# Optimization experiments

Hardware: AMD Instinct MI355X
Metric: run time of the kernel (lower is better)

Reference implementation:

```python
import jax, jax.numpy as jnp
import numpy as np

S, B, K = 64, 16, 512
QD, KD, A = 512, 512, 256


def setup_inputs() -> dict:
    key = jax.random.key(0)
    ks = jax.random.split(key, 10)
    inv_q = 1.0 / np.sqrt(QD)
    inv_k = 1.0 / np.sqrt(KD)
    inv_a = 1.0 / np.sqrt(A)
    return {
        "queries": jax.random.normal(ks[0], (S, B, QD), dtype=jnp.float32),
        "keys": jax.random.normal(ks[1], (B, K, KD), dtype=jnp.float32),
        "null_mask": jax.random.randint(ks[2], (B, K), 0, 2).astype(jnp.bool_),
        # nn.Linear params (PyTorch layout: weight (out, in), bias (out,))
        "Ww": jax.random.uniform(ks[3], (A, QD), jnp.float32, -inv_q, inv_q),
        "Wb": jax.random.uniform(ks[4], (A,), jnp.float32, -inv_q, inv_q),
        "Uw": jax.random.uniform(ks[5], (A, KD), jnp.float32, -inv_k, inv_k),
        "Ub": jax.random.uniform(ks[6], (A,), jnp.float32, -inv_k, inv_k),
        "vw": jax.random.uniform(ks[7], (1, A), jnp.float32, -inv_a, inv_a),
        "vb": jax.random.uniform(ks[8], (1,), jnp.float32, -inv_a, inv_a),
    }


def reference(queries, keys, null_mask, Ww, Wb, Uw, Ub, vw, vb):
    # t_query: (S, B, A); t_key: (B, K, A)
    t_query = jnp.einsum("sbq,aq->sba", queries, Ww) + Wb
    t_key = jnp.einsum("bkd,ad->bka", keys, Uw) + Ub
    # broadcast add -> (S, B, K, A), tanh, project with v -> alpha (S, B, K)
    h = jnp.tanh(t_query[:, :, None, :] + t_key[None, :, :, :])
    alpha = jnp.einsum("sbka,a->sbk", h, vw[0]) + vb[0]
    alpha = jnp.where(null_mask[None, :, :], -jnp.inf, alpha)
    att_weight = jax.nn.softmax(alpha, axis=2)  # (S, B, K)
    # bmm(att_weight^T, keys)^T -> (S, B, KD)
    attened_keys = jnp.einsum("sbk,bkd->sbd", att_weight, keys)
    return attened_keys, alpha
```

## Files before the change

kernel.cpp:

```cpp
#include <hip/hip_runtime.h>
#include <math.h>

#define S_DIM 64
#define B_DIM 16
#define K_DIM 512
#define QD_DIM 512
#define A_DIM 256

#define NEG_BIG (-3.0e38f)

#define SC 2.8853900817779268f

#define TQ_OFF 262144
#define W_WS_OFF ((size_t)2359296)

typedef __attribute__((ext_vector_type(8))) short short8v;
typedef __attribute__((ext_vector_type(4))) float f32x4;

static __device__ __forceinline__ uint2 pack_hi4(float4 v) {
    unsigned x0 = __float_as_uint(v.x), x1 = __float_as_uint(v.y),
             x2 = __float_as_uint(v.z), x3 = __float_as_uint(v.w);
    uint2 r;
    r.x = (x1 & 0xffff0000u) | (x0 >> 16);
    r.y = (x3 & 0xffff0000u) | (x2 >> 16);
    return r;
}
static __device__ __forceinline__ uint2 pack_lo4(float4 v) {
    float l0 = v.x - __uint_as_float(__float_as_uint(v.x) & 0xffff0000u);
    float l1 = v.y - __uint_as_float(__float_as_uint(v.y) & 0xffff0000u);
    float l2 = v.z - __uint_as_float(__float_as_uint(v.z) & 0xffff0000u);
    float l3 = v.w - __uint_as_float(__float_as_uint(v.w) & 0xffff0000u);
    unsigned y0 = __float_as_uint(l0), y1 = __float_as_uint(l1),
             y2 = __float_as_uint(l2), y3 = __float_as_uint(l3);
    uint2 r;
    r.x = (y1 & 0xffff0000u) | (y0 >> 16);
    r.y = (y3 & 0xffff0000u) | (y2 >> 16);
    return r;
}

__global__ __launch_bounds__(256) void lin_mfma(
    const float* __restrict__ queries, const float* __restrict__ keys,
    const float* __restrict__ Ww, const float* __restrict__ Wb,
    const float* __restrict__ Uw, const float* __restrict__ Ub,
    float* __restrict__ t_ws)
{
    __shared__ unsigned short Ah[64][40], Al[64][40], Bh[64][40], Bl[64][40];

    const int bx = blockIdx.x;
    const bool isQ = (bx < 64);
    int mt, nt;
    if (isQ) { mt = bx >> 2; nt = bx & 3; }
    else     { int t = bx - 64; mt = t >> 7; nt = t & 127; }

    const float* __restrict__ Abase = isQ ? queries : Uw;
    const float* __restrict__ Bbase = isQ ? Ww : keys;
    const size_t Aoff = (size_t)(mt * 64) * 512;
    const size_t Boff = (size_t)(nt * 64) * 512;

    const int tid  = threadIdx.x;
    const int srow = tid >> 2;
    const int scol = (tid & 3) << 3;
    const int lane = tid & 63, wid = tid >> 6;
    const int wm = (wid >> 1) << 5, wn = (wid & 1) << 5;
    const int fr  = lane & 15;
    const int fkb = (lane >> 4) << 3;

    f32x4 acc[2][2] = {};

    const float* Ap = Abase + Aoff + (size_t)srow * 512 + scol;
    const float* Bp = Bbase + Boff + (size_t)srow * 512 + scol;

    float4 ra0 = *(const float4*)(Ap);
    float4 ra1 = *(const float4*)(Ap + 4);
    float4 rb0 = *(const float4*)(Bp);
    float4 rb1 = *(const float4*)(Bp + 4);

    for (int ks = 0; ks < 16; ++ks) {
        uint2 ah0 = pack_hi4(ra0), ah1 = pack_hi4(ra1);
        uint2 al0 = pack_lo4(ra0), al1 = pack_lo4(ra1);
        uint2 bh0 = pack_hi4(rb0), bh1 = pack_hi4(rb1);
        uint2 bl0 = pack_lo4(rb0), bl1 = pack_lo4(rb1);
        __syncthreads();
        { uint4 v = {ah0.x, ah0.y, ah1.x, ah1.y}; *(uint4*)&Ah[srow][scol] = v; }
        { uint4 v = {al0.x, al0.y, al1.x, al1.y}; *(uint4*)&Al[srow][scol] = v; }
        { uint4 v = {bh0.x, bh0.y, bh1.x, bh1.y}; *(uint4*)&Bh[srow][scol] = v; }
        { uint4 v = {bl0.x, bl0.y, bl1.x, bl1.y}; *(uint4*)&Bl[srow][scol] = v; }
        __syncthreads();
        if (ks < 15) {
            const int o = (ks + 1) * 32;
            ra0 = *(const float4*)(Ap + o);
            ra1 = *(const float4*)(Ap + o + 4);
            rb0 = *(const float4*)(Bp + o);
            rb1 = *(const float4*)(Bp + o + 4);
        }
        short8v bhv[2], blv[2];
        #pragma unroll
        for (int j = 0; j < 2; ++j) {
            bhv[j] = *(const short8v*)&Bh[wn + j * 16 + fr][fkb];
            blv[j] = *(const short8v*)&Bl[wn + j * 16 + fr][fkb];
        }
        #pragma unroll
        for (int i = 0; i < 2; ++i) {
            short8v ah = *(const short8v*)&Ah[wm + i * 16 + fr][fkb];
            short8v al = *(const short8v*)&Al[wm + i * 16 + fr][fkb];
            #pragma unroll
            for (int j = 0; j < 2; ++j) {
                acc[i][j] = __builtin_amdgcn_mfma_f32_16x16x32_bf16(ah, bhv[j], acc[i][j], 0, 0, 0);
                acc[i][j] = __builtin_amdgcn_mfma_f32_16x16x32_bf16(ah, blv[j], acc[i][j], 0, 0, 0);
                acc[i][j] = __builtin_amdgcn_mfma_f32_16x16x32_bf16(al, bhv[j], acc[i][j], 0, 0, 0);
            }
        }
    }

    const int crow = (lane >> 4) << 2;
    if (isQ) {
        #pragma unroll
        for (int j = 0; j < 2; ++j) {
            const int a_col = nt * 64 + wn + j * 16 + fr;
            const float bias = Wb[a_col];
            #pragma unroll
            for (int i = 0; i < 2; ++i)
                #pragma unroll
                for (int r = 0; r < 4; ++r) {
                    const int m = mt * 64 + wm + i * 16 + crow + r;
                    t_ws[(size_t)m * 256 + a_col] = SC * (acc[i][j][r] + bias);
                }
        }
    } else {
        #pragma unroll
        for (int i = 0; i < 2; ++i)
            #pragma unroll
            for (int r = 0; r < 4; ++r) {
                const int a = mt * 64 + wm + i * 16 + crow + r;
                const float bias = Ub[a];
                #pragma unroll
                for (int j = 0; j < 2; ++j) {
                    const int n = nt * 64 + wn + j * 16 + fr;
                    t_ws[TQ_OFF + (size_t)(n >> 9) * 131072 + (size_t)a * 512 + (n & 511)]
                        = SC * (acc[i][j][r] + bias);
                }
            }
    }
}

__global__ __launch_bounds__(256) void alpha_kernel(
    const float* __restrict__ t_ws, const float* __restrict__ vw,
    const float* __restrict__ vb, const unsigned char* __restrict__ mask,
    float* __restrict__ alpha_out, float* __restrict__ w_ws)
{
    __shared__ float2 pv[256];
    __shared__ float redv[4], red_m[4], red_s[4];

    const int bid = blockIdx.x;
    const int b = bid >> 6;
    const int s = bid & 63;
    const int tid = threadIdx.x;
    const int lane = tid & 63, wid = tid >> 6;

    const float myvw = vw[tid];
    float2 p0; p0.x = t_ws[(size_t)(s * B_DIM + b) * A_DIM + tid]; p0.y = myvw;
    pv[tid] = p0;

    float sv = myvw;
    #pragma unroll
    for (int o = 32; o > 0; o >>= 1) sv += __shfl_xor(sv, o);
    if (lane == 0) redv[wid] = sv;
    __syncthreads();
    const float sumvw = redv[0] + redv[1] + redv[2] + redv[3];

    const float* __restrict__ tk = t_ws + TQ_OFF + (size_t)b * 131072;
    const int k2 = tid * 2;

    float acc0 = 0.f, acc1 = 0.f;
    #pragma unroll 8
    for (int a = 0; a < A_DIM; ++a) {
        float2 tv = *(const float2*)&tk[(size_t)a * 512 + k2];
        float2 p = pv[a];
        float x0 = p.x + tv.x;
        float x1 = p.x + tv.y;
        float r0 = __builtin_amdgcn_rcpf(exp2f(x0) + 1.0f);
        float r1 = __builtin_amdgcn_rcpf(exp2f(x1) + 1.0f);
        acc0 = fmaf(p.y, r0, acc0);
        acc1 = fmaf(p.y, r1, acc1);
    }

    const float base = sumvw + vb[0];
    float a0 = base - 2.0f * acc0;
    float a1 = base - 2.0f * acc1;
    const unsigned char* mrow = mask + b * K_DIM;
    if (mrow[k2])     a0 = NEG_BIG;
    if (mrow[k2 + 1]) a1 = NEG_BIG;

    *(float2*)&alpha_out[(size_t)(s * B_DIM + b) * K_DIM + k2] = make_float2(a0, a1);

    float m = fmaxf(a0, a1);
    #pragma unroll
    for (int o = 32; o > 0; o >>= 1) m = fmaxf(m, __shfl_xor(m, o));
    if (lane == 0) red_m[wid] = m;
    __syncthreads();
    const float mx = fmaxf(fmaxf(red_m[0], red_m[1]), fmaxf(red_m[2], red_m[3]));

    float e0 = __expf(a0 - mx);
    float e1 = __expf(a1 - mx);
    float ssum = e0 + e1;
    #pragma unroll
    for (int o = 32; o > 0; o >>= 1) ssum += __shfl_xor(ssum, o);
    if (lane == 0) red_s[wid] = ssum;
    __syncthreads();
    const float inv = 1.0f / (red_s[0] + red_s[1] + red_s[2] + red_s[3]);

    *(float2*)&w_ws[(size_t)(b * S_DIM + s) * K_DIM + k2] = make_float2(e0 * inv, e1 * inv);
}

__global__ __launch_bounds__(256) void att_kernel(
    const float* __restrict__ w_ws, const float* __restrict__ keys,
    float* __restrict__ out_att)
{
    __shared__ float wt[16][68];
    __shared__ float kt[64][64];

    const int d0g = blockIdx.x * 64;
    const int s0  = blockIdx.y * 16;
    const int b   = blockIdx.z;
    const int tid = threadIdx.x;

    const int sL = tid >> 4;
    const int dc = (tid & 15) << 2;

    float acc[4] = {};

    for (int k0 = 0; k0 < K_DIM; k0 += 64) {
        __syncthreads();
        *(float4*)&wt[sL][dc] =
            *(const float4*)&w_ws[(size_t)(b * S_DIM + s0 + sL) * K_DIM + k0 + dc];
        #pragma unroll
        for (int rr = 0; rr < 4; ++rr) {
            const int kr = (tid >> 4) + rr * 16;
            *(float4*)&kt[kr][dc] =
                *(const float4*)&keys[((size_t)b * K_DIM + k0 + kr) * QD_DIM + d0g + dc];
        }
        __syncthreads();
        #pragma unroll
        for (int kk = 0; kk < 64; kk += 4) {
            float4 wv = *(const float4*)&wt[sL][kk];
            float wr[4] = {wv.x, wv.y, wv.z, wv.w};
            #pragma unroll
            for (int u = 0; u < 4; ++u) {
                float4 kv = *(const float4*)&kt[kk + u][dc];
                acc[0] = fmaf(wr[u], kv.x, acc[0]);
                acc[1] = fmaf(wr[u], kv.y, acc[1]);
                acc[2] = fmaf(wr[u], kv.z, acc[2]);
                acc[3] = fmaf(wr[u], kv.w, acc[3]);
            }
        }
    }

    float4 o = {acc[0], acc[1], acc[2], acc[3]};
    *(float4*)&out_att[(size_t)((s0 + sL) * B_DIM + b) * QD_DIM + d0g + dc] = o;
}

extern "C" void kernel_launch(void* const* d_in, const int* in_sizes, int n_in,
                              void* d_out, int out_size, void* d_ws, size_t ws_size,
                              hipStream_t stream) {
    const float* queries = (const float*)d_in[0];
    const float* keys    = (const float*)d_in[1];
    const unsigned char* mask = (const unsigned char*)d_in[2];
    const float* Ww = (const float*)d_in[3];
    const float* Wb = (const float*)d_in[4];
    const float* Uw = (const float*)d_in[5];
    const float* Ub = (const float*)d_in[6];
    const float* vw = (const float*)d_in[7];
    const float* vb = (const float*)d_in[8];

    float* out_att   = (float*)d_out;
    float* out_alpha = (float*)d_out + (size_t)S_DIM * B_DIM * QD_DIM;

    float* t_ws = (float*)d_ws;
    float* w_ws = t_ws + W_WS_OFF;

    lin_mfma<<<576, 256, 0, stream>>>(queries, keys, Ww, Wb, Uw, Ub, t_ws);

    alpha_kernel<<<S_DIM * B_DIM, 256, 0, stream>>>(t_ws, vw, vb, mask,
                                                    out_alpha, w_ws);

    dim3 gC(QD_DIM / 64, S_DIM / 16, B_DIM);
    att_kernel<<<gC, 256, 0, stream>>>(w_ws, keys, out_att);
}
```

Measured before the change: 160.1 us.

## Pre-split inputs into bf16 hi/lo once and process two queries per alpha block

```diff
diff --git a/kernel.cpp b/kernel.cpp
--- a/kernel.cpp
+++ b/kernel.cpp
@@ -11,8 +11,11 @@
 
 #define SC 2.8853900817779268f
 
-#define TQ_OFF 262144
+#define TK_OFF 262144
 #define W_WS_OFF ((size_t)2359296)
+#define CONV_F32_OFF ((size_t)2883584)
+#define CONV_ROWS 9728
+#define LO_USHORT_OFF ((size_t)CONV_ROWS * 512)
 
 typedef __attribute__((ext_vector_type(8))) short short8v;
 typedef __attribute__((ext_vector_type(4))) float f32x4;
@@ -38,10 +41,34 @@
     return r;
 }
 
+__global__ __launch_bounds__(256) void conv_kernel(
+    const float* __restrict__ q, const float* __restrict__ k,
+    const float* __restrict__ ww, const float* __restrict__ uw,
+    unsigned short* __restrict__ hi, unsigned short* __restrict__ lo)
+{
+    const int idx = blockIdx.x * 256 + threadIdx.x;
+    const int row = idx >> 6;
+    const int c   = (idx & 63) << 3;
+
+    const float* __restrict__ src;
+    if (row < 1024)      src = q  + (size_t)row * 512;
+    else if (row < 9216) src = k  + (size_t)(row - 1024) * 512;
+    else if (row < 9472) src = ww + (size_t)(row - 9216) * 512;
+    else                 src = uw + (size_t)(row - 9472) * 512;
+
+    float4 v0 = *(const float4*)(src + c);
+    float4 v1 = *(const float4*)(src + c + 4);
+    uint2 h0 = pack_hi4(v0), h1 = pack_hi4(v1);
+    uint2 l0 = pack_lo4(v0), l1 = pack_lo4(v1);
+    uint4 H = {h0.x, h0.y, h1.x, h1.y};
+    uint4 L = {l0.x, l0.y, l1.x, l1.y};
+    *(uint4*)&hi[(size_t)row * 512 + c] = H;
+    *(uint4*)&lo[(size_t)row * 512 + c] = L;
+}
+
 __global__ __launch_bounds__(256) void lin_mfma(
-    const float* __restrict__ queries, const float* __restrict__ keys,
-    const float* __restrict__ Ww, const float* __restrict__ Wb,
-    const float* __restrict__ Uw, const float* __restrict__ Ub,
+    const unsigned short* __restrict__ hi, const unsigned short* __restrict__ lo,
+    const float* __restrict__ Wb, const float* __restrict__ Ub,
     float* __restrict__ t_ws)
 {
     __shared__ unsigned short Ah[64][40], Al[64][40], Bh[64][40], Bl[64][40];
@@ -52,10 +79,8 @@
     if (isQ) { mt = bx >> 2; nt = bx & 3; }
     else     { int t = bx - 64; mt = t >> 7; nt = t & 127; }
 
-    const float* __restrict__ Abase = isQ ? queries : Uw;
-    const float* __restrict__ Bbase = isQ ? Ww : keys;
-    const size_t Aoff = (size_t)(mt * 64) * 512;
-    const size_t Boff = (size_t)(nt * 64) * 512;
+    const int aro = isQ ? (mt * 64) : (9472 + mt * 64);
+    const int bro = isQ ? (9216 + nt * 64) : (1024 + nt * 64);
 
     const int tid  = threadIdx.x;
     const int srow = tid >> 2;
@@ -67,31 +92,29 @@
 
     f32x4 acc[2][2] = {};
 
-    const float* Ap = Abase + Aoff + (size_t)srow * 512 + scol;
-    const float* Bp = Bbase + Boff + (size_t)srow * 512 + scol;
-
-    float4 ra0 = *(const float4*)(Ap);
-    float4 ra1 = *(const float4*)(Ap + 4);
-    float4 rb0 = *(const float4*)(Bp);
-    float4 rb1 = *(const float4*)(Bp + 4);
+    const unsigned short* pAh = hi + (size_t)(aro + srow) * 512 + scol;
+    const unsigned short* pAl = lo + (size_t)(aro + srow) * 512 + scol;
+    const unsigned short* pBh = hi + (size_t)(bro + srow) * 512 + scol;
+    const unsigned short* pBl = lo + (size_t)(bro + srow) * 512 + scol;
+
+    uint4 rah = *(const uint4*)(pAh);
+    uint4 ral = *(const uint4*)(pAl);
+    uint4 rbh = *(const uint4*)(pBh);
+    uint4 rbl = *(const uint4*)(pBl);
 
     for (int ks = 0; ks < 16; ++ks) {
-        uint2 ah0 = pack_hi4(ra0), ah1 = pack_hi4(ra1);
-        uint2 al0 = pack_lo4(ra0), al1 = pack_lo4(ra1);
-        uint2 bh0 = pack_hi4(rb0), bh1 = pack_hi4(rb1);
-        uint2 bl0 = pack_lo4(rb0), bl1 = pack_lo4(rb1);
         __syncthreads();
-        { uint4 v = {ah0.x, ah0.y, ah1.x, ah1.y}; *(uint4*)&Ah[srow][scol] = v; }
-        { uint4 v = {al0.x, al0.y, al1.x, al1.y}; *(uint4*)&Al[srow][scol] = v; }
-        { uint4 v = {bh0.x, bh0.y, bh1.x, bh1.y}; *(uint4*)&Bh[srow][scol] = v; }
-        { uint4 v = {bl0.x, bl0.y, bl1.x, bl1.y}; *(uint4*)&Bl[srow][scol] = v; }
+        *(uint4*)&Ah[srow][scol] = rah;
+        *(uint4*)&Al[srow][scol] = ral;
+        *(uint4*)&Bh[srow][scol] = rbh;
+        *(uint4*)&Bl[srow][scol] = rbl;
         __syncthreads();
         if (ks < 15) {
             const int o = (ks + 1) * 32;
-            ra0 = *(const float4*)(Ap + o);
-            ra1 = *(const float4*)(Ap + o + 4);
-            rb0 = *(const float4*)(Bp + o);
-            rb1 = *(const float4*)(Bp + o + 4);
+            rah = *(const uint4*)(pAh + o);
+            ral = *(const uint4*)(pAl + o);
+            rbh = *(const uint4*)(pBh + o);
+            rbl = *(const uint4*)(pBl + o);
         }
         short8v bhv[2], blv[2];
         #pragma unroll
@@ -136,7 +159,7 @@
                 #pragma unroll
                 for (int j = 0; j < 2; ++j) {
                     const int n = nt * 64 + wn + j * 16 + fr;
-                    t_ws[TQ_OFF + (size_t)(n >> 9) * 131072 + (size_t)a * 512 + (n & 511)]
+                    t_ws[TK_OFF + (size_t)(n >> 9) * 131072 + (size_t)a * 512 + (n & 511)]
                         = SC * (acc[i][j][r] + bias);
                 }
             }
@@ -148,68 +171,86 @@
     const float* __restrict__ vb, const unsigned char* __restrict__ mask,
     float* __restrict__ alpha_out, float* __restrict__ w_ws)
 {
-    __shared__ float2 pv[256];
-    __shared__ float redv[4], red_m[4], red_s[4];
+    __shared__ float4 pv[256];
+    __shared__ float red[5][4];
 
     const int bid = blockIdx.x;
-    const int b = bid >> 6;
-    const int s = bid & 63;
+    const int b  = bid >> 5;
+    const int sp = (bid & 31) << 1;
     const int tid = threadIdx.x;
     const int lane = tid & 63, wid = tid >> 6;
 
     const float myvw = vw[tid];
-    float2 p0; p0.x = t_ws[(size_t)(s * B_DIM + b) * A_DIM + tid]; p0.y = myvw;
-    pv[tid] = p0;
+    {
+        float4 p;
+        p.x = t_ws[(size_t)(sp * B_DIM + b) * A_DIM + tid];
+        p.y = t_ws[(size_t)((sp + 1) * B_DIM + b) * A_DIM + tid];
+        p.z = myvw; p.w = 0.f;
+        pv[tid] = p;
+    }
 
     float sv = myvw;
     #pragma unroll
     for (int o = 32; o > 0; o >>= 1) sv += __shfl_xor(sv, o);
-    if (lane == 0) redv[wid] = sv;
+    if (lane == 0) red[0][wid] = sv;
     __syncthreads();
-    const float sumvw = redv[0] + redv[1] + redv[2] + redv[3];
-
-    const float* __restrict__ tk = t_ws + TQ_OFF + (size_t)b * 131072;
+    const float sumvw = red[0][0] + red[0][1] + red[0][2] + red[0][3];
+
+    const float* __restrict__ tk = t_ws + TK_OFF + (size_t)b * 131072;
     const int k2 = tid * 2;
 
-    float acc0 = 0.f, acc1 = 0.f;
-    #pragma unroll 8
+    float acc00 = 0.f, acc01 = 0.f, acc10 = 0.f, acc11 = 0.f;
+    #pragma unroll 4
     for (int a = 0; a < A_DIM; ++a) {
         float2 tv = *(const float2*)&tk[(size_t)a * 512 + k2];
-        float2 p = pv[a];
-        float x0 = p.x + tv.x;
-        float x1 = p.x + tv.y;
-        float r0 = __builtin_amdgcn_rcpf(exp2f(x0) + 1.0f);
-        float r1 = __builtin_amdgcn_rcpf(exp2f(x1) + 1.0f);
-        acc0 = fmaf(p.y, r0, acc0);
-        acc1 = fmaf(p.y, r1, acc1);
+        float4 p = pv[a];
+        float e00 = __builtin_amdgcn_exp2f(p.x + tv.x);
+        float e01 = __builtin_amdgcn_exp2f(p.x + tv.y);
+        float e10 = __builtin_amdgcn_exp2f(p.y + tv.x);
+        float e11 = __builtin_amdgcn_exp2f(p.y + tv.y);
+        acc00 = fmaf(p.z, __builtin_amdgcn_rcpf(e00 + 1.0f), acc00);
+        acc01 = fmaf(p.z, __builtin_amdgcn_rcpf(e01 + 1.0f), acc01);
+        acc10 = fmaf(p.z, __builtin_amdgcn_rcpf(e10 + 1.0f), acc10);
+        acc11 = fmaf(p.z, __builtin_amdgcn_rcpf(e11 + 1.0f), acc11);
     }
 
     const float base = sumvw + vb[0];
-    float a0 = base - 2.0f * acc0;
-    float a1 = base - 2.0f * acc1;
+    float a00 = base - 2.0f * acc00, a01 = base - 2.0f * acc01;
+    float a10 = base - 2.0f * acc10, a11 = base - 2.0f * acc11;
     const unsigned char* mrow = mask + b * K_DIM;
-    if (mrow[k2])     a0 = NEG_BIG;
-    if (mrow[k2 + 1]) a1 = NEG_BIG;
-
-    *(float2*)&alpha_out[(size_t)(s * B_DIM + b) * K_DIM + k2] = make_float2(a0, a1);
-
-    float m = fmaxf(a0, a1);
+    const bool m0 = mrow[k2] != 0, m1 = mrow[k2 + 1] != 0;
+    if (m0) { a00 = NEG_BIG; a10 = NEG_BIG; }
+    if (m1) { a01 = NEG_BIG; a11 = NEG_BIG; }
+
+    *(float2*)&alpha_out[(size_t)(sp * B_DIM + b) * K_DIM + k2] = make_float2(a00, a01);
+    *(float2*)&alpha_out[(size_t)((sp + 1) * B_DIM + b) * K_DIM + k2] = make_float2(a10, a11);
+
+    float mm0 = fmaxf(a00, a01), mm1 = fmaxf(a10, a11);
     #pragma unroll
-    for (int o = 32; o > 0; o >>= 1) m = fmaxf(m, __shfl_xor(m, o));
-    if (lane == 0) red_m[wid] = m;
+    for (int o = 32; o > 0; o >>= 1) {
+        mm0 = fmaxf(mm0, __shfl_xor(mm0, o));
+        mm1 = fmaxf(mm1, __shfl_xor(mm1, o));
+    }
+    if (lane == 0) { red[1][wid] = mm0; red[2][wid] = mm1; }
     __syncthreads();
-    const float mx = fmaxf(fmaxf(red_m[0], red_m[1]), fmaxf(red_m[2], red_m[3]));
-
-    float e0 = __expf(a0 - mx);
-    float e1 = __expf(a1 - mx);
-    float ssum = e0 + e1;
+    const float mx0 = fmaxf(fmaxf(red[1][0], red[1][1]), fmaxf(red[1][2], red[1][3]));
+    const float mx1 = fmaxf(fmaxf(red[2][0], red[2][1]), fmaxf(red[2][2], red[2][3]));
+
+    float e00 = __expf(a00 - mx0), e01 = __expf(a01 - mx0);
+    float e10 = __expf(a10 - mx1), e11 = __expf(a11 - mx1);
+    float s0 = e00 + e01, s1 = e10 + e11;
     #pragma unroll
-    for (int o = 32; o > 0; o >>= 1) ssum += __shfl_xor(ssum, o);
-    if (lane == 0) red_s[wid] = ssum;
+    for (int o = 32; o > 0; o >>= 1) {
+        s0 += __shfl_xor(s0, o);
+        s1 += __shfl_xor(s1, o);
+    }
+    if (lane == 0) { red[3][wid] = s0; red[4][wid] = s1; }
     __syncthreads();
-    const float inv = 1.0f / (red_s[0] + red_s[1] + red_s[2] + red_s[3]);
-
-    *(float2*)&w_ws[(size_t)(b * S_DIM + s) * K_DIM + k2] = make_float2(e0 * inv, e1 * inv);
+    const float inv0 = 1.0f / (red[3][0] + red[3][1] + red[3][2] + red[3][3]);
+    const float inv1 = 1.0f / (red[4][0] + red[4][1] + red[4][2] + red[4][3]);
+
+    *(float2*)&w_ws[(size_t)(b * S_DIM + sp) * K_DIM + k2] = make_float2(e00 * inv0, e01 * inv0);
+    *(float2*)&w_ws[(size_t)(b * S_DIM + sp + 1) * K_DIM + k2] = make_float2(e10 * inv1, e11 * inv1);
 }
 
 __global__ __launch_bounds__(256) void att_kernel(
@@ -277,11 +318,15 @@
 
     float* t_ws = (float*)d_ws;
     float* w_ws = t_ws + W_WS_OFF;
-
-    lin_mfma<<<576, 256, 0, stream>>>(queries, keys, Ww, Wb, Uw, Ub, t_ws);
-
-    alpha_kernel<<<S_DIM * B_DIM, 256, 0, stream>>>(t_ws, vw, vb, mask,
-                                                    out_alpha, w_ws);
+    unsigned short* hi = (unsigned short*)(t_ws + CONV_F32_OFF);
+    unsigned short* lo = hi + LO_USHORT_OFF;
+
+    conv_kernel<<<2432, 256, 0, stream>>>(queries, keys, Ww, Uw, hi, lo);
+
+    lin_mfma<<<576, 256, 0, stream>>>(hi, lo, Wb, Ub, t_ws);
+
+    alpha_kernel<<<512, 256, 0, stream>>>(t_ws, vw, vb, mask,
+                                          out_alpha, w_ws);
 
     dim3 gC(QD_DIM / 64, S_DIM / 16, B_DIM);
     att_kernel<<<gC, 256, 0, stream>>>(w_ws, keys, out_att);
```

After: 152.3 us. 1.05x faster.
